# Performance work log

Measured on AMD Instinct MI355X. Metric: run time of the kernel, lower is better.

## Reference

```python
import jax, jax.numpy as jnp
import numpy as np

INPUT = 28
HID = 64
OUT = 10


def setup_inputs() -> dict:
    key = jax.random.key(0)
    ks = jax.random.split(key, 8)
    s_ih = 1.0 / np.sqrt(HID)
    x = jax.random.normal(ks[0], (16384, 28, INPUT), dtype=jnp.float32)
    # PyTorch LSTM params: gate order (i, f, g, o), each block of size HID
    W_ih = jax.random.uniform(ks[1], (4 * HID, INPUT), jnp.float32, -s_ih, s_ih)
    W_hh = jax.random.uniform(ks[2], (4 * HID, HID), jnp.float32, -s_ih, s_ih)
    b_ih = jax.random.uniform(ks[3], (4 * HID,), jnp.float32, -s_ih, s_ih)
    b_hh = jax.random.uniform(ks[4], (4 * HID,), jnp.float32, -s_ih, s_ih)
    s_fc = 1.0 / np.sqrt(HID)
    W_fc = jax.random.uniform(ks[5], (OUT, HID), jnp.float32, -s_fc, s_fc)
    b_fc = jax.random.uniform(ks[6], (OUT,), jnp.float32, -s_fc, s_fc)
    return {"x": x, "W_ih": W_ih, "W_hh": W_hh, "b_ih": b_ih, "b_hh": b_hh,
            "W_fc": W_fc, "b_fc": b_fc}


def reference(x, W_ih, W_hh, b_ih, b_hh, W_fc, b_fc):
    B = x.shape[0]
    # Precompute input projections for all timesteps in one big GEMM: [T, B, 4H]
    x_proj = jnp.einsum('bti,gi->tbg', x, W_ih) + (b_ih + b_hh)

    def step(carry, xp_t):
        h, c = carry
        gates = xp_t + h @ W_hh.T  # [B, 4H]
        i, f, g, o = jnp.split(gates, 4, axis=-1)
        i = jax.nn.sigmoid(i)
        f = jax.nn.sigmoid(f)
        g = jnp.tanh(g)
        o = jax.nn.sigmoid(o)
        c = f * c + i * g
        h = o * jnp.tanh(c)
        return (h, c), None

    h0 = jnp.zeros((B, HID), dtype=x.dtype)
    c0 = jnp.zeros((B, HID), dtype=x.dtype)
    (h_last, _), _ = jax.lax.scan(step, (h0, c0), x_proj)
    # fc on the last timestep's hidden state (== output[:, -1, :])
    return h_last @ W_fc.T + b_fc
```

## Files before the change

### kernel.cpp

```cpp
#include <hip/hip_runtime.h>
#include <hip/hip_bf16.h>


namespace {
constexpr int B_TOT   = 16384;
constexpr int T_STEPS = 28;
constexpr int IN_DIM  = 28;
constexpr int HID     = 64;
constexpr int OUT_DIM = 10;
constexpr int ROWS    = 16;
constexpr int THREADS = 256;
constexpr int KP      = 104;
constexpr int XROW    = T_STEPS * IN_DIM;
constexpr int WS_ELEMS = 48 * 64 * 8;
}

typedef __attribute__((ext_vector_type(8))) short short8v;
typedef __attribute__((ext_vector_type(4))) short short4v;
typedef __attribute__((ext_vector_type(4))) float float4v;

__device__ __forceinline__ short f2bf_cold(float f) {
  union { float f; unsigned u; } v; v.f = f;
  unsigned r = v.u + 0x7FFFu + ((v.u >> 16) & 1u);
  return (short)(r >> 16);
}
__device__ __forceinline__ float bf2f(short s) {
  union { unsigned u; float f; } v; v.u = ((unsigned)(unsigned short)s) << 16;
  return v.f;
}
__device__ __forceinline__ unsigned pk2(float a, float b) {
  __hip_bfloat162 h = __float22bfloat162_rn(float2{a, b});
  union { __hip_bfloat162 h; unsigned u; } cv; cv.h = h; return cv.u;
}

__global__ void lstm_prep(const float* __restrict__ W_ih,
                          const float* __restrict__ W_hh,
                          const float* __restrict__ b_ih,
                          const float* __restrict__ b_hh,
                          unsigned short* __restrict__ ws) {
  int idx = blockIdx.x * blockDim.x + threadIdx.x;
  if (idx >= WS_ELEMS) return;
  int j  = idx & 7;
  int l  = (idx >> 3) & 63;
  int fk = idx >> 9;
  int kc = fk % 3;
  int mt = fk / 3;
  int m  = 16 * mt + (l & 15);
  int unit = m >> 2, type = m & 3;
  int g  = type * 64 + unit;
  int k  = kc * 32 + (l >> 4) * 8 + j;
  float v = 0.0f;
  if (k < IN_DIM)        v = W_ih[g * IN_DIM + k];
  else if (k == IN_DIM)  v = b_ih[g] + b_hh[g];
  else if (k >= 32) {
    int p = k - 32;
    int u = 16 * (p >> 4) + 4 * (p & 3) + ((p >> 2) & 3);
    v = W_hh[g * HID + u];
  }
  v *= (type == 2) ? 2.8853900817779268f : 1.4426950408889634f;
  ws[idx] = (unsigned short)f2bf_cold(v);
}

__global__ __attribute__((amdgpu_flat_work_group_size(THREADS, THREADS),
                          amdgpu_waves_per_eu(4, 4)))
void lstm_mfma9(const float* __restrict__ x,
                const unsigned short* __restrict__ wfrag,
                const float* __restrict__ W_fc,
                const float* __restrict__ b_fc, float* __restrict__ out) {
  __shared__ short hs[2][ROWS][KP];

  const int tid  = threadIdx.x;
  const int lane = tid & 63;
  const int w    = tid >> 6;
  const int l15  = lane & 15;
  const int q    = lane >> 4;
  const int b0   = blockIdx.x * ROWS;

  short8v a[4][3];
#pragma unroll
  for (int i = 0; i < 4; ++i)
#pragma unroll
    for (int kc = 0; kc < 3; ++kc)
      a[i][kc] = *(const short8v*)&wfrag[((((4 * w + i) * 3) + kc) * 64 + lane) * 8];

  for (int idx = tid; idx < 2 * ROWS * KP; idx += THREADS) (&hs[0][0][0])[idx] = 0;
  __syncthreads();
  if (tid < 2 * ROWS) hs[tid >> 4][tid & 15][IN_DIM] = (short)0x3F80;

  const bool stager = (lane < 28);
  const int  s  = w * 28 + lane;
  const int  sr = s / 7;
  const int  sc = s - 7 * sr;
  const float* xptr = x + (size_t)(b0 + sr) * XROW + sc * 4;

  float4 xfly = {0.f, 0.f, 0.f, 0.f};
  if (stager) {
    float4 x0 = *(const float4*)xptr;
    short4v sv;
    unsigned plo = pk2(x0.x, x0.y), phi = pk2(x0.z, x0.w);
    sv[0] = (short)(plo & 0xFFFF); sv[1] = (short)(plo >> 16);
    sv[2] = (short)(phi & 0xFFFF); sv[3] = (short)(phi >> 16);
    *(short4v*)&hs[0][sr][sc * 4] = sv;
    xfly = *(const float4*)(xptr + 1 * IN_DIM);
  }
  __syncthreads();

  float c_state[4] = {0.f, 0.f, 0.f, 0.f};

  for (int t = 0; t < T_STEPS; ++t) {
    const int cur = t & 1, nxt = cur ^ 1;

    short8v bf0 = *(const short8v*)&hs[cur][l15][q * 8];
    short8v bf1 = *(const short8v*)&hs[cur][l15][32 + q * 8];
    short8v bf2 = *(const short8v*)&hs[cur][l15][64 + q * 8];

    if (stager) {
      if (t + 1 < T_STEPS) {
        short4v sv;
        unsigned plo = pk2(xfly.x, xfly.y), phi = pk2(xfly.z, xfly.w);
        sv[0] = (short)(plo & 0xFFFF); sv[1] = (short)(plo >> 16);
        sv[2] = (short)(phi & 0xFFFF); sv[3] = (short)(phi >> 16);
        *(short4v*)&hs[nxt][sr][sc * 4] = sv;
      }
      if (t + 2 < T_STEPS)
        xfly = *(const float4*)(xptr + (t + 2) * IN_DIM);
    }

    const float4v zero4 = {0.f, 0.f, 0.f, 0.f};
    float4v acc[4];
#pragma unroll
    for (int i = 0; i < 4; ++i)
      acc[i] = __builtin_amdgcn_mfma_f32_16x16x32_bf16(a[i][0], bf0, zero4, 0, 0, 0);
#pragma unroll
    for (int i = 0; i < 4; ++i)
      acc[i] = __builtin_amdgcn_mfma_f32_16x16x32_bf16(a[i][1], bf1, acc[i], 0, 0, 0);
#pragma unroll
    for (int i = 0; i < 4; ++i)
      acc[i] = __builtin_amdgcn_mfma_f32_16x16x32_bf16(a[i][2], bf2, acc[i], 0, 0, 0);

    float hv[4];
#pragma unroll
    for (int i = 0; i < 4; ++i) {
      float4v g4 = acc[i];
      float Ei = __builtin_amdgcn_exp2f(-g4[0]);
      float Ef = __builtin_amdgcn_exp2f(-g4[1]);
      float Eg = __builtin_amdgcn_exp2f(-g4[2]);
      float di = 1.0f + Ei, df = 1.0f + Ef, dg = 1.0f + Eg;
      float t1 = di * df;
      float r1 = __builtin_amdgcn_rcpf(t1 * dg);
      float iv = r1 * (df * dg);
      float fv = r1 * (di * dg);
      float gnum = fmaf(-Eg, 2.8853900817779268f, 2.8853900817779268f);
      float gv = (r1 * t1) * gnum;
      float cn = fmaf(fv, c_state[i], iv * gv);
      c_state[i] = cn;
      float ct = fminf(fmaxf(cn, -44.0f), 44.0f);
      float Eo = __builtin_amdgcn_exp2f(-g4[3]);
      float Ec = __builtin_amdgcn_exp2f(-ct);
      float dn = 1.0f + Eo, dc = 1.0f + Ec;
      float r2 = __builtin_amdgcn_rcpf(dn * dc);
      float ov = r2 * dc;
      float tc = (r2 * dn) * (1.0f - Ec);
      hv[i] = ov * tc;
    }
    unsigned p01 = pk2(hv[0], hv[1]);
    unsigned p23 = pk2(hv[2], hv[3]);
    union { unsigned u[2]; short4v s; } pw;
    pw.u[0] = p01; pw.u[1] = p23;
    *(short4v*)&hs[nxt][l15][32 + 16 * w + 4 * q] = pw.s;

    __syncthreads();
  }

  if (tid < ROWS * OUT_DIM) {
    const int r = tid / OUT_DIM;
    const int o = tid - r * OUT_DIM;
    float sacc = b_fc[o];
#pragma unroll
    for (int p = 0; p < HID; ++p) {
      const int u = 16 * (p >> 4) + 4 * (p & 3) + ((p >> 2) & 3);
      sacc += bf2f(hs[0][r][32 + p]) * W_fc[o * HID + u];
    }
    out[(b0 + r) * OUT_DIM + o] = sacc;
  }
}

extern "C" void kernel_launch(void* const* d_in, const int* in_sizes, int n_in,
                              void* d_out, int out_size, void* d_ws, size_t ws_size,
                              hipStream_t stream) {
  const float* x    = (const float*)d_in[0];
  const float* W_ih = (const float*)d_in[1];
  const float* W_hh = (const float*)d_in[2];
  const float* b_ih = (const float*)d_in[3];
  const float* b_hh = (const float*)d_in[4];
  const float* W_fc = (const float*)d_in[5];
  const float* b_fc = (const float*)d_in[6];
  float* out = (float*)d_out;
  unsigned short* ws = (unsigned short*)d_ws;

  lstm_prep<<<(WS_ELEMS + 255) / 256, 256, 0, stream>>>(W_ih, W_hh, b_ih, b_hh, ws);

  dim3 grid(B_TOT / ROWS);
  dim3 block(THREADS);
  lstm_mfma9<<<grid, block, 0, stream>>>(x, ws, W_fc, b_fc, out);
}
```

Baseline: 134.2 us.

## Give each wave its own 16-row batch tile and drop block barriers

Previously the four waves of a block split the 256 gate rows of one 16-row batch tile and synchronised through shared memory with __syncthreads every timestep. Now each wave keeps all 16 weight fragments in registers and runs its own 16 batch rows independently. Each wave loads its x inputs straight into the MFMA B operand and reuses a private LDS slice for h, so the block barrier and the x staging path are removed. The cost is far higher register pressure (occupancy set to one wave per EU) and a longer serial chain of MFMAs and transcendental ops per wave, which means less latency hiding across waves.

```diff
diff --git a/kernel.cpp b/kernel.cpp
--- a/kernel.cpp
+++ b/kernel.cpp
@@ -8,9 +8,9 @@
 constexpr int IN_DIM  = 28;
 constexpr int HID     = 64;
 constexpr int OUT_DIM = 10;
-constexpr int ROWS    = 16;
+constexpr int RPW     = 16;
 constexpr int THREADS = 256;
-constexpr int KP      = 104;
+constexpr int HP      = 72;
 constexpr int XROW    = T_STEPS * IN_DIM;
 constexpr int WS_ELEMS = 48 * 64 * 8;
 }
@@ -18,6 +18,7 @@
 typedef __attribute__((ext_vector_type(8))) short short8v;
 typedef __attribute__((ext_vector_type(4))) short short4v;
 typedef __attribute__((ext_vector_type(4))) float float4v;
+typedef __attribute__((ext_vector_type(4))) int   int4v;
 
 __device__ __forceinline__ short f2bf_cold(float f) {
   union { float f; unsigned u; } v; v.f = f;
@@ -54,7 +55,7 @@
   else if (k == IN_DIM)  v = b_ih[g] + b_hh[g];
   else if (k >= 32) {
     int p = k - 32;
-    int u = 16 * (p >> 4) + 4 * (p & 3) + ((p >> 2) & 3);
+    int u = 4 * (p & 15) + (p >> 4);
     v = W_hh[g * HID + u];
   }
   v *= (type == 2) ? 2.8853900817779268f : 1.4426950408889634f;
@@ -62,85 +63,72 @@
 }
 
 __global__ __attribute__((amdgpu_flat_work_group_size(THREADS, THREADS),
-                          amdgpu_waves_per_eu(4, 4)))
-void lstm_mfma9(const float* __restrict__ x,
-                const unsigned short* __restrict__ wfrag,
-                const float* __restrict__ W_fc,
-                const float* __restrict__ b_fc, float* __restrict__ out) {
-  __shared__ short hs[2][ROWS][KP];
+                          amdgpu_waves_per_eu(1, 1)))
+void lstm_mfma11(const float* __restrict__ x,
+                 const unsigned short* __restrict__ wfrag,
+                 const float* __restrict__ W_fc,
+                 const float* __restrict__ b_fc, float* __restrict__ out) {
+  __shared__ short hs[4][RPW][HP];
 
   const int tid  = threadIdx.x;
   const int lane = tid & 63;
   const int w    = tid >> 6;
   const int l15  = lane & 15;
   const int q    = lane >> 4;
-  const int b0   = blockIdx.x * ROWS;
+  const int row  = blockIdx.x * (4 * RPW) + 16 * w + l15;
 
-  short8v a[4][3];
+  short8v a[16][3];
 #pragma unroll
-  for (int i = 0; i < 4; ++i)
+  for (int i = 0; i < 16; ++i)
 #pragma unroll
     for (int kc = 0; kc < 3; ++kc)
-      a[i][kc] = *(const short8v*)&wfrag[((((4 * w + i) * 3) + kc) * 64 + lane) * 8];
+      a[i][kc] = *(const short8v*)&wfrag[(((i * 3) + kc) * 64 + lane) * 8];
 
-  for (int idx = tid; idx < 2 * ROWS * KP; idx += THREADS) (&hs[0][0][0])[idx] = 0;
-  __syncthreads();
-  if (tid < 2 * ROWS) hs[tid >> 4][tid & 15][IN_DIM] = (short)0x3F80;
-
-  const bool stager = (lane < 28);
-  const int  s  = w * 28 + lane;
-  const int  sr = s / 7;
-  const int  sc = s - 7 * sr;
-  const float* xptr = x + (size_t)(b0 + sr) * XROW + sc * 4;
-
-  float4 xfly = {0.f, 0.f, 0.f, 0.f};
-  if (stager) {
-    float4 x0 = *(const float4*)xptr;
-    short4v sv;
-    unsigned plo = pk2(x0.x, x0.y), phi = pk2(x0.z, x0.w);
-    sv[0] = (short)(plo & 0xFFFF); sv[1] = (short)(plo >> 16);
-    sv[2] = (short)(phi & 0xFFFF); sv[3] = (short)(phi >> 16);
-    *(short4v*)&hs[0][sr][sc * 4] = sv;
-    xfly = *(const float4*)(xptr + 1 * IN_DIM);
-  }
+  for (int idx = tid; idx < 4 * RPW * HP; idx += THREADS) (&hs[0][0][0])[idx] = 0;
   __syncthreads();
 
-  float c_state[4] = {0.f, 0.f, 0.f, 0.f};
+  short (*hsw)[HP] = hs[w];
+
+  const float* xrow = x + (size_t)row * XROW + q * 8;
+  float4 lo = *(const float4*)xrow;
+  float4 hi = {0.f, 0.f, 0.f, 0.f};
+  if (q < 3) hi = *(const float4*)(xrow + 4);
+  else       hi.x = 1.0f;
+
+  float c_state[16];
+#pragma unroll
+  for (int i = 0; i < 16; ++i) c_state[i] = 0.0f;
 
   for (int t = 0; t < T_STEPS; ++t) {
-    const int cur = t & 1, nxt = cur ^ 1;
+    int4v xi;
+    xi[0] = pk2(lo.x, lo.y); xi[1] = pk2(lo.z, lo.w);
+    xi[2] = pk2(hi.x, hi.y); xi[3] = pk2(hi.z, hi.w);
+    union { int4v i; short8v s; } xb; xb.i = xi;
 
-    short8v bf0 = *(const short8v*)&hs[cur][l15][q * 8];
-    short8v bf1 = *(const short8v*)&hs[cur][l15][32 + q * 8];
-    short8v bf2 = *(const short8v*)&hs[cur][l15][64 + q * 8];
+    short8v hf1 = *(const short8v*)&hsw[l15][8 * q];
+    short8v hf2 = *(const short8v*)&hsw[l15][32 + 8 * q];
 
-    if (stager) {
-      if (t + 1 < T_STEPS) {
-        short4v sv;
-        unsigned plo = pk2(xfly.x, xfly.y), phi = pk2(xfly.z, xfly.w);
-        sv[0] = (short)(plo & 0xFFFF); sv[1] = (short)(plo >> 16);
-        sv[2] = (short)(phi & 0xFFFF); sv[3] = (short)(phi >> 16);
-        *(short4v*)&hs[nxt][sr][sc * 4] = sv;
-      }
-      if (t + 2 < T_STEPS)
-        xfly = *(const float4*)(xptr + (t + 2) * IN_DIM);
+    if (t + 1 < T_STEPS) {
+      const float* xp = xrow + (t + 1) * IN_DIM;
+      lo = *(const float4*)xp;
+      if (q < 3) hi = *(const float4*)(xp + 4);
     }
 
     const float4v zero4 = {0.f, 0.f, 0.f, 0.f};
-    float4v acc[4];
+    float4v acc[16];
 #pragma unroll
-    for (int i = 0; i < 4; ++i)
-      acc[i] = __builtin_amdgcn_mfma_f32_16x16x32_bf16(a[i][0], bf0, zero4, 0, 0, 0);
+    for (int i = 0; i < 16; ++i)
+      acc[i] = __builtin_amdgcn_mfma_f32_16x16x32_bf16(a[i][0], xb.s, zero4, 0, 0, 0);
 #pragma unroll
-    for (int i = 0; i < 4; ++i)
-      acc[i] = __builtin_amdgcn_mfma_f32_16x16x32_bf16(a[i][1], bf1, acc[i], 0, 0, 0);
+    for (int i = 0; i < 16; ++i)
+      acc[i] = __builtin_amdgcn_mfma_f32_16x16x32_bf16(a[i][1], hf1, acc[i], 0, 0, 0);
 #pragma unroll
-    for (int i = 0; i < 4; ++i)
-      acc[i] = __builtin_amdgcn_mfma_f32_16x16x32_bf16(a[i][2], bf2, acc[i], 0, 0, 0);
+    for (int i = 0; i < 16; ++i)
+      acc[i] = __builtin_amdgcn_mfma_f32_16x16x32_bf16(a[i][2], hf2, acc[i], 0, 0, 0);
 
-    float hv[4];
+    float hv[16];
 #pragma unroll
-    for (int i = 0; i < 4; ++i) {
+    for (int i = 0; i < 16; ++i) {
       float4v g4 = acc[i];
       float Ei = __builtin_amdgcn_exp2f(-g4[0]);
       float Ef = __builtin_amdgcn_exp2f(-g4[1]);
@@ -163,25 +151,26 @@
       float tc = (r2 * dn) * (1.0f - Ec);
       hv[i] = ov * tc;
     }
-    unsigned p01 = pk2(hv[0], hv[1]);
-    unsigned p23 = pk2(hv[2], hv[3]);
-    union { unsigned u[2]; short4v s; } pw;
-    pw.u[0] = p01; pw.u[1] = p23;
-    *(short4v*)&hs[nxt][l15][32 + 16 * w + 4 * q] = pw.s;
 
-    __syncthreads();
+    union { unsigned u[8]; short8v s[2]; } pw;
+#pragma unroll
+    for (int e = 0; e < 8; ++e) pw.u[e] = pk2(hv[2 * e], hv[2 * e + 1]);
+    *(short8v*)&hsw[l15][16 * q]     = pw.s[0];
+    *(short8v*)&hsw[l15][16 * q + 8] = pw.s[1];
   }
 
-  if (tid < ROWS * OUT_DIM) {
-    const int r = tid / OUT_DIM;
-    const int o = tid - r * OUT_DIM;
-    float sacc = b_fc[o];
 #pragma unroll
-    for (int p = 0; p < HID; ++p) {
-      const int u = 16 * (p >> 4) + 4 * (p & 3) + ((p >> 2) & 3);
-      sacc += bf2f(hs[0][r][32 + p]) * W_fc[o * HID + u];
+  for (int c = 0; c < 3; ++c) {
+    const int o = q + 4 * c;
+    if (o < OUT_DIM) {
+      float sacc = b_fc[o];
+#pragma unroll
+      for (int p = 0; p < HID; ++p) {
+        const int u = 4 * (p & 15) + (p >> 4);
+        sacc += bf2f(hsw[l15][p]) * W_fc[o * HID + u];
+      }
+      out[(size_t)row * OUT_DIM + o] = sacc;
     }
-    out[(b0 + r) * OUT_DIM + o] = sacc;
   }
 }
 
@@ -200,7 +189,7 @@
 
   lstm_prep<<<(WS_ELEMS + 255) / 256, 256, 0, stream>>>(W_ih, W_hh, b_ih, b_hh, ws);
 
-  dim3 grid(B_TOT / ROWS);
+  dim3 grid(B_TOT / (4 * RPW));
   dim3 block(THREADS);
-  lstm_mfma9<<<grid, block, 0, stream>>>(x, ws, W_fc, b_fc, out);
+  lstm_mfma11<<<grid, block, 0, stream>>>(x, ws, W_fc, b_fc, out);
 }
```

New measurement: 143.9 us. 7.2% more time.

## Process two independent batch cohorts per block to interleave MFMA and activation work

Applied to the files above, without the earlier changes.

Each block now handles two 16-row cohorts instead of one, reusing the register-resident weight fragments across both and issuing both cohorts' MFMA chains before their activations. This halves the grid and the per-step barrier count per row, and gives the scheduler independent work to hide MFMA and transcendental latency within the serial recurrence. In exchange the block uses more registers and LDS, waves_per_eu drops from 4 to 2, and there are fewer blocks to hide latency across the device.

```diff
diff --git a/kernel.cpp b/kernel.cpp
--- a/kernel.cpp
+++ b/kernel.cpp
@@ -8,7 +8,8 @@
 constexpr int IN_DIM  = 28;
 constexpr int HID     = 64;
 constexpr int OUT_DIM = 10;
-constexpr int ROWS    = 16;
+constexpr int RPC     = 16;
+constexpr int NCOH    = 2;
 constexpr int THREADS = 256;
 constexpr int KP      = 104;
 constexpr int XROW    = T_STEPS * IN_DIM;
@@ -61,20 +62,44 @@
   ws[idx] = (unsigned short)f2bf_cold(v);
 }
 
+__device__ __forceinline__ void act_tuple(const float4v g4, float& c,
+                                          float& hv) {
+  float Ei = __builtin_amdgcn_exp2f(-g4[0]);
+  float Ef = __builtin_amdgcn_exp2f(-g4[1]);
+  float Eg = __builtin_amdgcn_exp2f(-g4[2]);
+  float di = 1.0f + Ei, df = 1.0f + Ef, dg = 1.0f + Eg;
+  float t1 = di * df;
+  float r1 = __builtin_amdgcn_rcpf(t1 * dg);
+  float iv = r1 * (df * dg);
+  float fv = r1 * (di * dg);
+  float gnum = fmaf(-Eg, 2.8853900817779268f, 2.8853900817779268f);
+  float gv = (r1 * t1) * gnum;
+  float cn = fmaf(fv, c, iv * gv);
+  c = cn;
+  float ct = fminf(fmaxf(cn, -44.0f), 44.0f);
+  float Eo = __builtin_amdgcn_exp2f(-g4[3]);
+  float Ec = __builtin_amdgcn_exp2f(-ct);
+  float dn = 1.0f + Eo, dc = 1.0f + Ec;
+  float r2 = __builtin_amdgcn_rcpf(dn * dc);
+  float ov = r2 * dc;
+  float tc = (r2 * dn) * (1.0f - Ec);
+  hv = ov * tc;
+}
+
 __global__ __attribute__((amdgpu_flat_work_group_size(THREADS, THREADS),
-                          amdgpu_waves_per_eu(4, 4)))
-void lstm_mfma9(const float* __restrict__ x,
-                const unsigned short* __restrict__ wfrag,
-                const float* __restrict__ W_fc,
-                const float* __restrict__ b_fc, float* __restrict__ out) {
-  __shared__ short hs[2][ROWS][KP];
+                          amdgpu_waves_per_eu(2, 2)))
+void lstm_mfma12(const float* __restrict__ x,
+                 const unsigned short* __restrict__ wfrag,
+                 const float* __restrict__ W_fc,
+                 const float* __restrict__ b_fc, float* __restrict__ out) {
+  __shared__ short hs[NCOH][2][RPC][KP];
 
   const int tid  = threadIdx.x;
   const int lane = tid & 63;
   const int w    = tid >> 6;
   const int l15  = lane & 15;
   const int q    = lane >> 4;
-  const int b0   = blockIdx.x * ROWS;
+  const int b0   = blockIdx.x * (NCOH * RPC);
 
   short8v a[4][3];
 #pragma unroll
@@ -83,14 +108,19 @@
     for (int kc = 0; kc < 3; ++kc)
       a[i][kc] = *(const short8v*)&wfrag[((((4 * w + i) * 3) + kc) * 64 + lane) * 8];
 
-  for (int idx = tid; idx < 2 * ROWS * KP; idx += THREADS) (&hs[0][0][0])[idx] = 0;
+  for (int idx = tid; idx < NCOH * 2 * RPC * KP; idx += THREADS)
+    (&hs[0][0][0][0])[idx] = 0;
   __syncthreads();
-  if (tid < 2 * ROWS) hs[tid >> 4][tid & 15][IN_DIM] = (short)0x3F80;
-
-  const bool stager = (lane < 28);
-  const int  s  = w * 28 + lane;
+  if (tid < NCOH * 2 * RPC) {
+    int coh = tid >> 5, buf = (tid >> 4) & 1, r = tid & 15;
+    hs[coh][buf][r][IN_DIM] = (short)0x3F80;
+  }
+
+  const int  s  = w * 56 + lane;
+  const bool stager = (lane < 56);
   const int  sr = s / 7;
   const int  sc = s - 7 * sr;
+  const int  scoh = sr >> 4, srow = sr & 15;
   const float* xptr = x + (size_t)(b0 + sr) * XROW + sc * 4;
 
   float4 xfly = {0.f, 0.f, 0.f, 0.f};
@@ -100,19 +130,22 @@
     unsigned plo = pk2(x0.x, x0.y), phi = pk2(x0.z, x0.w);
     sv[0] = (short)(plo & 0xFFFF); sv[1] = (short)(plo >> 16);
     sv[2] = (short)(phi & 0xFFFF); sv[3] = (short)(phi >> 16);
-    *(short4v*)&hs[0][sr][sc * 4] = sv;
+    *(short4v*)&hs[scoh][0][srow][sc * 4] = sv;
     xfly = *(const float4*)(xptr + 1 * IN_DIM);
   }
   __syncthreads();
 
-  float c_state[4] = {0.f, 0.f, 0.f, 0.f};
+  float c_state[NCOH][4] = {{0.f, 0.f, 0.f, 0.f}, {0.f, 0.f, 0.f, 0.f}};
 
   for (int t = 0; t < T_STEPS; ++t) {
     const int cur = t & 1, nxt = cur ^ 1;
 
-    short8v bf0 = *(const short8v*)&hs[cur][l15][q * 8];
-    short8v bf1 = *(const short8v*)&hs[cur][l15][32 + q * 8];
-    short8v bf2 = *(const short8v*)&hs[cur][l15][64 + q * 8];
+    short8v bfA0 = *(const short8v*)&hs[0][cur][l15][q * 8];
+    short8v bfA1 = *(const short8v*)&hs[0][cur][l15][32 + q * 8];
+    short8v bfA2 = *(const short8v*)&hs[0][cur][l15][64 + q * 8];
+    short8v bfB0 = *(const short8v*)&hs[1][cur][l15][q * 8];
+    short8v bfB1 = *(const short8v*)&hs[1][cur][l15][32 + q * 8];
+    short8v bfB2 = *(const short8v*)&hs[1][cur][l15][64 + q * 8];
 
     if (stager) {
       if (t + 1 < T_STEPS) {
@@ -120,68 +153,71 @@
         unsigned plo = pk2(xfly.x, xfly.y), phi = pk2(xfly.z, xfly.w);
         sv[0] = (short)(plo & 0xFFFF); sv[1] = (short)(plo >> 16);
         sv[2] = (short)(phi & 0xFFFF); sv[3] = (short)(phi >> 16);
-        *(short4v*)&hs[nxt][sr][sc * 4] = sv;
+        *(short4v*)&hs[scoh][nxt][srow][sc * 4] = sv;
       }
       if (t + 2 < T_STEPS)
         xfly = *(const float4*)(xptr + (t + 2) * IN_DIM);
     }
 
     const float4v zero4 = {0.f, 0.f, 0.f, 0.f};
-    float4v acc[4];
-#pragma unroll
-    for (int i = 0; i < 4; ++i)
-      acc[i] = __builtin_amdgcn_mfma_f32_16x16x32_bf16(a[i][0], bf0, zero4, 0, 0, 0);
-#pragma unroll
-    for (int i = 0; i < 4; ++i)
-      acc[i] = __builtin_amdgcn_mfma_f32_16x16x32_bf16(a[i][1], bf1, acc[i], 0, 0, 0);
-#pragma unroll
-    for (int i = 0; i < 4; ++i)
-      acc[i] = __builtin_amdgcn_mfma_f32_16x16x32_bf16(a[i][2], bf2, acc[i], 0, 0, 0);
-
-    float hv[4];
-#pragma unroll
-    for (int i = 0; i < 4; ++i) {
-      float4v g4 = acc[i];
-      float Ei = __builtin_amdgcn_exp2f(-g4[0]);
-      float Ef = __builtin_amdgcn_exp2f(-g4[1]);
-      float Eg = __builtin_amdgcn_exp2f(-g4[2]);
-      float di = 1.0f + Ei, df = 1.0f + Ef, dg = 1.0f + Eg;
-      float t1 = di * df;
-      float r1 = __builtin_amdgcn_rcpf(t1 * dg);
-      float iv = r1 * (df * dg);
-      float fv = r1 * (di * dg);
-      float gnum = fmaf(-Eg, 2.8853900817779268f, 2.8853900817779268f);
-      float gv = (r1 * t1) * gnum;
-      float cn = fmaf(fv, c_state[i], iv * gv);
-      c_state[i] = cn;
-      float ct = fminf(fmaxf(cn, -44.0f), 44.0f);
-      float Eo = __builtin_amdgcn_exp2f(-g4[3]);
-      float Ec = __builtin_amdgcn_exp2f(-ct);
-      float dn = 1.0f + Eo, dc = 1.0f + Ec;
-      float r2 = __builtin_amdgcn_rcpf(dn * dc);
-      float ov = r2 * dc;
-      float tc = (r2 * dn) * (1.0f - Ec);
-      hv[i] = ov * tc;
-    }
-    unsigned p01 = pk2(hv[0], hv[1]);
-    unsigned p23 = pk2(hv[2], hv[3]);
-    union { unsigned u[2]; short4v s; } pw;
-    pw.u[0] = p01; pw.u[1] = p23;
-    *(short4v*)&hs[nxt][l15][32 + 16 * w + 4 * q] = pw.s;
+    float4v accA[4], accB[4];
+#pragma unroll
+    for (int i = 0; i < 4; ++i)
+      accA[i] = __builtin_amdgcn_mfma_f32_16x16x32_bf16(a[i][0], bfA0, zero4, 0, 0, 0);
+#pragma unroll
+    for (int i = 0; i < 4; ++i)
+      accA[i] = __builtin_amdgcn_mfma_f32_16x16x32_bf16(a[i][1], bfA1, accA[i], 0, 0, 0);
+#pragma unroll
+    for (int i = 0; i < 4; ++i)
+      accA[i] = __builtin_amdgcn_mfma_f32_16x16x32_bf16(a[i][2], bfA2, accA[i], 0, 0, 0);
+#pragma unroll
+    for (int i = 0; i < 4; ++i)
+      accB[i] = __builtin_amdgcn_mfma_f32_16x16x32_bf16(a[i][0], bfB0, zero4, 0, 0, 0);
+#pragma unroll
+    for (int i = 0; i < 4; ++i)
+      accB[i] = __builtin_amdgcn_mfma_f32_16x16x32_bf16(a[i][1], bfB1, accB[i], 0, 0, 0);
+#pragma unroll
+    for (int i = 0; i < 4; ++i)
+      accB[i] = __builtin_amdgcn_mfma_f32_16x16x32_bf16(a[i][2], bfB2, accB[i], 0, 0, 0);
+
+    {
+      float hv[4];
+#pragma unroll
+      for (int i = 0; i < 4; ++i) act_tuple(accA[i], c_state[0][i], hv[i]);
+      unsigned p01 = pk2(hv[0], hv[1]);
+      unsigned p23 = pk2(hv[2], hv[3]);
+      union { unsigned u[2]; short4v s4; } pw;
+      pw.u[0] = p01; pw.u[1] = p23;
+      *(short4v*)&hs[0][nxt][l15][32 + 16 * w + 4 * q] = pw.s4;
+    }
+    {
+      float hv[4];
+#pragma unroll
+      for (int i = 0; i < 4; ++i) act_tuple(accB[i], c_state[1][i], hv[i]);
+      unsigned p01 = pk2(hv[0], hv[1]);
+      unsigned p23 = pk2(hv[2], hv[3]);
+      union { unsigned u[2]; short4v s4; } pw;
+      pw.u[0] = p01; pw.u[1] = p23;
+      *(short4v*)&hs[1][nxt][l15][32 + 16 * w + 4 * q] = pw.s4;
+    }
 
     __syncthreads();
   }
 
-  if (tid < ROWS * OUT_DIM) {
-    const int r = tid / OUT_DIM;
-    const int o = tid - r * OUT_DIM;
-    float sacc = b_fc[o];
-#pragma unroll
-    for (int p = 0; p < HID; ++p) {
-      const int u = 16 * (p >> 4) + 4 * (p & 3) + ((p >> 2) & 3);
-      sacc += bf2f(hs[0][r][32 + p]) * W_fc[o * HID + u];
-    }
-    out[(b0 + r) * OUT_DIM + o] = sacc;
+  for (int base = 0; base < NCOH * RPC * OUT_DIM; base += THREADS) {
+    int idx = base + tid;
+    if (idx < NCOH * RPC * OUT_DIM) {
+      const int r = idx / OUT_DIM;
+      const int o = idx - r * OUT_DIM;
+      const int coh = r >> 4, rr = r & 15;
+      float sacc = b_fc[o];
+#pragma unroll
+      for (int p = 0; p < HID; ++p) {
+        const int u = 16 * (p >> 4) + 4 * (p & 3) + ((p >> 2) & 3);
+        sacc += bf2f(hs[coh][0][rr][32 + p]) * W_fc[o * HID + u];
+      }
+      out[(size_t)(b0 + r) * OUT_DIM + o] = sacc;
+    }
   }
 }
 
@@ -200,7 +236,7 @@
 
   lstm_prep<<<(WS_ELEMS + 255) / 256, 256, 0, stream>>>(W_ih, W_hh, b_ih, b_hh, ws);
 
-  dim3 grid(B_TOT / ROWS);
+  dim3 grid(B_TOT / (NCOH * RPC));
   dim3 block(THREADS);
-  lstm_mfma9<<<grid, block, 0, stream>>>(x, ws, W_fc, b_fc, out);
-}
+  lstm_mfma12<<<grid, block, 0, stream>>>(x, ws, W_fc, b_fc, out);
+}
```

After: 132.6 us. Within noise of the previous version (-1.2%).
